# Kernel optimization log

Measured on AMD Instinct MI355X. Metric: run time of the kernel, lower is better.

Reference implementation:

```python
import jax, jax.numpy as jnp
import numpy as np

INFEAT = 4096
OUTFEAT = 11008
TOKENS = 2048


def setup_inputs() -> dict:
    key = jax.random.key(0)
    k1, k2, k3, k4, k5 = jax.random.split(key, 5)
    x = jax.random.normal(k1, (TOKENS, INFEAT), dtype=jnp.float32)
    # Random uint8 int-weights, packed 4-per-uint32 exactly like pack():
    # word = w1 | w2<<8 | w3<<16 | w4<<24, rows grouped along infeatures.
    wbytes = jax.random.randint(k2, (INFEAT // 4, 4, OUTFEAT), 0, 256, dtype=jnp.int32).astype(jnp.uint32)
    qweight = (wbytes[:, 0] | (wbytes[:, 1] << 8) | (wbytes[:, 2] << 16) | (wbytes[:, 3] << 24))
    qweight = qweight.astype(jnp.int32)  # same bit pattern as uint32 buffer
    scales = (jax.random.uniform(k3, (OUTFEAT,), dtype=jnp.float32) * 0.01 + 1e-4)
    zeros = jax.random.randint(k4, (OUTFEAT,), 0, 256, dtype=jnp.int32)  # uint8 zero points
    bias = jax.random.normal(k5, (OUTFEAT,), dtype=jnp.float32) * 0.01
    return {"x": x, "qweight": qweight, "scales": scales, "zeros": zeros, "bias": bias}


def _dequant(qweight, scales, zeros):
    q = qweight.astype(jnp.uint32)  # [INFEAT//4, OUTFEAT]
    b0 = (q & 0xFF)
    b1 = ((q >> 8) & 0xFF)
    b2 = ((q >> 16) & 0xFF)
    b3 = ((q >> 24) & 0xFF)
    w_int = jnp.stack([b0, b1, b2, b3], axis=1).reshape(-1, q.shape[-1])  # [INFEAT, OUTFEAT]
    # pack(): int = round(w/scale) + zero  =>  w = (int - zero) * scale (per output channel)
    return (w_int.astype(jnp.float32) - zeros.astype(jnp.float32)[None, :]) * scales[None, :]


def reference(x, qweight, scales, zeros, bias):
    w = _dequant(qweight, scales, zeros)          # [INFEAT, OUTFEAT]
    return x @ w + bias[None, :]                  # [TOKENS, OUTFEAT]
```

## Files before the change

kernel.cpp:

```cpp
#include <hip/hip_runtime.h>
#include <hip/hip_bf16.h>

#define INFEAT 4096
#define OUTFEAT 11008
#define TOKENS 2048

typedef int v4i __attribute__((ext_vector_type(4)));
typedef __bf16 bf16_t;
typedef bf16_t bf16x4 __attribute__((ext_vector_type(4)));
typedef bf16_t bf16x8 __attribute__((ext_vector_type(8)));
typedef float f32x4 __attribute__((ext_vector_type(4)));

__device__ __forceinline__ void async_copy16(const void* g, void* l) {
    __builtin_amdgcn_global_load_lds((const __attribute__((address_space(1))) void*)g,
                                     (__attribute__((address_space(3))) void*)l,
                                     16, 0, 0);
}

__global__ __launch_bounds__(256) void quant_x(
    const float* __restrict__ x, unsigned int* __restrict__ xq,
    float* __restrict__ xscale, int* __restrict__ xsum)
{
    __shared__ float smax[4];
    __shared__ int ssum[4];
    const int row = blockIdx.x;
    const int tid = threadIdx.x;
    const int lane = tid & 63, wid = tid >> 6;
    const float* xr = x + (size_t)row * INFEAT;

    float4 v[4];
    #pragma unroll
    for (int i = 0; i < 4; ++i) v[i] = *(const float4*)&xr[tid * 16 + i * 4];

    float am = 0.f;
    #pragma unroll
    for (int i = 0; i < 4; ++i)
        am = fmaxf(am, fmaxf(fmaxf(fabsf(v[i].x), fabsf(v[i].y)),
                             fmaxf(fabsf(v[i].z), fabsf(v[i].w))));
    #pragma unroll
    for (int o = 32; o > 0; o >>= 1) am = fmaxf(am, __shfl_xor(am, o, 64));
    if (lane == 0) smax[wid] = am;
    __syncthreads();
    am = fmaxf(fmaxf(smax[0], smax[1]), fmaxf(smax[2], smax[3]));
    const float inv = am > 0.f ? 127.0f / am : 0.f;
    const float sc  = am > 0.f ? am / 127.0f : 0.f;

    int lsum = 0;
    unsigned int pk[4];
    #pragma unroll
    for (int i = 0; i < 4; ++i) {
        int q0 = (int)rintf(fminf(fmaxf(v[i].x * inv, -127.f), 127.f));
        int q1 = (int)rintf(fminf(fmaxf(v[i].y * inv, -127.f), 127.f));
        int q2 = (int)rintf(fminf(fmaxf(v[i].z * inv, -127.f), 127.f));
        int q3 = (int)rintf(fminf(fmaxf(v[i].w * inv, -127.f), 127.f));
        lsum += q0 + q1 + q2 + q3;
        pk[i] = (q0 & 255) | ((q1 & 255) << 8) | ((q2 & 255) << 16) | ((unsigned)(q3 & 255) << 24);
    }
    *(uint4*)&xq[(size_t)row * (INFEAT / 4) + tid * 4] = *(uint4*)pk;

    #pragma unroll
    for (int o = 32; o > 0; o >>= 1) lsum += __shfl_xor(lsum, o, 64);
    if (lane == 0) ssum[wid] = lsum;
    __syncthreads();
    if (tid == 0) {
        xsum[row] = ssum[0] + ssum[1] + ssum[2] + ssum[3];
        xscale[row] = sc;
    }
}

__global__ __launch_bounds__(256) void t_w(
    const unsigned int* __restrict__ qw, unsigned char* __restrict__ wt)
{
    __shared__ unsigned int Tw[64 * 64];
    const int n0 = blockIdx.x * 64;
    const int kp0 = blockIdx.y * 64;
    const int tn = threadIdx.x & 63;
    const int tk4 = threadIdx.x >> 6;

    #pragma unroll
    for (int it = 0; it < 16; ++it) {
        const int kp = tk4 * 16 + it;
        const unsigned int q = qw[(size_t)(kp0 + kp) * OUTFEAT + n0 + tn] ^ 0x80808080u;
        const int slot = (kp >> 2) ^ (tn & 15);
        Tw[tn * 64 + slot * 4 + (kp & 3)] = q;
    }
    __syncthreads();

    #pragma unroll
    for (int i = 0; i < 4; ++i) {
        const int flat = i * 256 + threadIdx.x;
        const int n = flat >> 4;
        const int c = flat & 15;
        uint4 v = *(const uint4*)&Tw[n * 64 + ((c ^ (n & 15)) * 4)];
        *(uint4*)&wt[(size_t)(n0 + n) * INFEAT + (size_t)kp0 * 4 + c * 16] = v;
    }
}

__global__ __launch_bounds__(256, 4) void q3gemm_i8(
    const unsigned char* __restrict__ xqb, const unsigned char* __restrict__ wt,
    const float* __restrict__ scales, const int* __restrict__ zeros,
    const float* __restrict__ bias, const float* __restrict__ xscale,
    const int* __restrict__ xsum, float* __restrict__ out)
{
    __shared__ unsigned char Als[128 * 128];
    __shared__ unsigned char Bls[128 * 128];

    const int tid = threadIdx.x;
    const int n0 = (blockIdx.x >> 4) * 128;
    const int m0 = (blockIdx.x & 15) * 128;

    const int wid = tid >> 6, lane = tid & 63;
    const int wm = (wid & 1) * 64, wn = (wid >> 1) * 64;
    const int lr = lane & 15, lq = lane >> 4;

    const int rb0  = wid * 32;
    const int rsub = lane >> 3;
    const int sl   = lane & 7;

    v4i acc[4][4];
    #pragma unroll
    for (int i = 0; i < 4; ++i)
        #pragma unroll
        for (int j = 0; j < 4; ++j)
            acc[i][j] = (v4i){0, 0, 0, 0};

    for (int kt = 0; kt < INFEAT / 128; ++kt) {
        const int k0 = kt * 128;

        #pragma unroll
        for (int p = 0; p < 4; ++p) {
            const int r = rb0 + p * 8 + rsub;
            const int s = sl ^ (r & 7);
            async_copy16(&xqb[(size_t)(m0 + r) * INFEAT + k0 + s * 16], Als + (rb0 + p * 8) * 128);
        }
        #pragma unroll
        for (int p = 0; p < 4; ++p) {
            const int r = rb0 + p * 8 + rsub;
            const int s = sl ^ (r & 7);
            async_copy16(&wt[(size_t)(n0 + r) * INFEAT + k0 + s * 16], Bls + (rb0 + p * 8) * 128);
        }

        __syncthreads();

        #pragma unroll
        for (int ks = 0; ks < 2; ++ks) {
            v4i af[4], bfv[4];
            #pragma unroll
            for (int t = 0; t < 4; ++t) {
                const int ra = wm + t * 16 + lr;
                const int pa = (ks * 4 + lq) ^ (ra & 7);
                af[t] = *(const v4i*)&Als[ra * 128 + pa * 16];
                const int rb = wn + t * 16 + lr;
                const int pb = (ks * 4 + lq) ^ (rb & 7);
                bfv[t] = *(const v4i*)&Bls[rb * 128 + pb * 16];
            }
            #pragma unroll
            for (int i = 0; i < 4; ++i)
                #pragma unroll
                for (int j = 0; j < 4; ++j)
                    acc[i][j] = __builtin_amdgcn_mfma_i32_16x16x64_i8(af[i], bfv[j], acc[i][j], 0, 0, 0);
        }

        __syncthreads();
    }

    #pragma unroll
    for (int j = 0; j < 4; ++j) {
        const int col = n0 + wn + j * 16 + lr;
        const float sn = scales[col];
        const int zi = 128 - zeros[col];
        const float bv = bias[col];
        #pragma unroll
        for (int i = 0; i < 4; ++i) {
            const int rb = m0 + wm + i * 16 + lq * 4;
            #pragma unroll
            for (int r = 0; r < 4; ++r) {
                const int tot = acc[i][j][r] + zi * xsum[rb + r];
                out[(size_t)(rb + r) * OUTFEAT + col] = xscale[rb + r] * sn * (float)tot + bv;
            }
        }
    }
}

#define LDSS 72
__global__ __launch_bounds__(256) void q3gemm_fb(
    const float* __restrict__ x, const unsigned int* __restrict__ qw,
    const float* __restrict__ scales, const int* __restrict__ zeros,
    const float* __restrict__ bias, float* __restrict__ out)
{
    __shared__ bf16_t Als[128 * LDSS];
    __shared__ bf16_t Bls[128 * LDSS];
    const int tid = threadIdx.x;
    const int m0 = blockIdx.y * 128;
    const int n0 = blockIdx.x * 128;
    const int bcol = tid & 127;
    const int bpr  = tid >> 7;
    const float scf = scales[n0 + bcol];
    const float nzs = (float)zeros[n0 + bcol] * scf;
    const int acolg = tid & 15;
    const int arow0 = tid >> 4;
    const int wid  = tid >> 6;
    const int lane = tid & 63;
    const int wm = (wid & 1) * 64;
    const int wn = (wid >> 1) * 64;
    const int lr = lane & 15;
    const int lq = lane >> 4;
    f32x4 acc[4][4];
    #pragma unroll
    for (int i = 0; i < 4; ++i)
        #pragma unroll
        for (int j = 0; j < 4; ++j) acc[i][j] = (f32x4)0.0f;
    for (int kt = 0; kt < INFEAT / 64; ++kt) {
        const int k0 = kt * 64;
        #pragma unroll
        for (int p = 0; p < 8; ++p) {
            const int row = arow0 + p * 16;
            const float4 v = *(const float4*)&x[(size_t)(m0 + row) * INFEAT + k0 + acolg * 4];
            bf16x4 b;
            b[0] = (bf16_t)v.x; b[1] = (bf16_t)v.y; b[2] = (bf16_t)v.z; b[3] = (bf16_t)v.w;
            *(bf16x4*)&Als[row * LDSS + acolg * 4] = b;
        }
        const int kp0 = k0 >> 2;
        #pragma unroll
        for (int it = 0; it < 8; ++it) {
            const int prel = it * 2 + bpr;
            const unsigned int q = qw[(size_t)(kp0 + prel) * OUTFEAT + n0 + bcol];
            bf16x4 b;
            b[0] = (bf16_t)((float)(q & 0xFFu)        * scf - nzs);
            b[1] = (bf16_t)((float)((q >> 8) & 0xFFu) * scf - nzs);
            b[2] = (bf16_t)((float)((q >> 16) & 0xFFu)* scf - nzs);
            b[3] = (bf16_t)((float)(q >> 24)          * scf - nzs);
            *(bf16x4*)&Bls[bcol * LDSS + prel * 4] = b;
        }
        __syncthreads();
        #pragma unroll
        for (int ks = 0; ks < 2; ++ks) {
            bf16x8 af[4], bfv[4];
            #pragma unroll
            for (int t = 0; t < 4; ++t) {
                af[t]  = *(const bf16x8*)&Als[(wm + t * 16 + lr) * LDSS + ks * 32 + lq * 8];
                bfv[t] = *(const bf16x8*)&Bls[(wn + t * 16 + lr) * LDSS + ks * 32 + lq * 8];
            }
            #pragma unroll
            for (int i = 0; i < 4; ++i)
                #pragma unroll
                for (int j = 0; j < 4; ++j)
                    acc[i][j] = __builtin_amdgcn_mfma_f32_16x16x32_bf16(af[i], bfv[j], acc[i][j], 0, 0, 0);
        }
        __syncthreads();
    }
    #pragma unroll
    for (int j = 0; j < 4; ++j) {
        const int col = n0 + wn + j * 16 + lr;
        const float bv = bias[col];
        #pragma unroll
        for (int i = 0; i < 4; ++i) {
            const int rbs = m0 + wm + i * 16 + lq * 4;
            #pragma unroll
            for (int r = 0; r < 4; ++r)
                out[(size_t)(rbs + r) * OUTFEAT + col] = acc[i][j][r] + bv;
        }
    }
}

extern "C" void kernel_launch(void* const* d_in, const int* in_sizes, int n_in,
                              void* d_out, int out_size, void* d_ws, size_t ws_size,
                              hipStream_t stream) {
    const float*        x      = (const float*)d_in[0];
    const unsigned int* qw     = (const unsigned int*)d_in[1];
    const float*        scales = (const float*)d_in[2];
    const int*          zeros  = (const int*)d_in[3];
    const float*        bias   = (const float*)d_in[4];
    float*              out    = (float*)d_out;

    const size_t wt_bytes = (size_t)OUTFEAT * INFEAT;
    const size_t xq_bytes = (size_t)TOKENS * INFEAT;
    const size_t need = wt_bytes + xq_bytes + TOKENS * (sizeof(float) + sizeof(int)) + 256;

    if (ws_size >= need) {
        unsigned char* wt = (unsigned char*)d_ws;
        unsigned int* xq  = (unsigned int*)((char*)d_ws + wt_bytes);
        float* xscale = (float*)((char*)d_ws + wt_bytes + xq_bytes);
        int*   xsum   = (int*)((char*)d_ws + wt_bytes + xq_bytes + TOKENS * sizeof(float));

        quant_x<<<dim3(TOKENS), dim3(256), 0, stream>>>(x, xq, xscale, xsum);
        t_w<<<dim3(OUTFEAT / 64, (INFEAT / 4) / 64), dim3(256), 0, stream>>>(qw, wt);
        q3gemm_i8<<<dim3((OUTFEAT / 128) * (TOKENS / 128)), dim3(256), 0, stream>>>(
            (const unsigned char*)xq, wt, scales, zeros, bias, xscale, xsum, out);
    } else {
        q3gemm_fb<<<dim3(OUTFEAT / 128, TOKENS / 128), dim3(256), 0, stream>>>(
            x, qw, scales, zeros, bias, out);
    }
}
```

Baseline: 297.6 us.

## Fuse prep kernels and triple-buffer a 256x128 int8 MFMA GEMM

Merges the activation quantization and weight transpose into one launch, and the transpose now reads with 16-byte loads. The int8 GEMM moves to 512-thread blocks with 256x128 tiles and a three-stage async global-to-LDS pipeline. K-steps are split into phases interleaved with prefetches, with explicit waitcnt, barriers and setprio. This aims to hide load latency and cut launch overhead, at the cost of much more LDS per block (144KB), lower occupancy and fragile hand-written synchronisation.

```diff
diff --git a/kernel.cpp b/kernel.cpp
--- a/kernel.cpp
+++ b/kernel.cpp
@@ -17,151 +17,227 @@
                                      16, 0, 0);
 }
 
-__global__ __launch_bounds__(256) void quant_x(
-    const float* __restrict__ x, unsigned int* __restrict__ xq,
-    float* __restrict__ xscale, int* __restrict__ xsum)
+__global__ __launch_bounds__(256) void prep(
+    const float* __restrict__ x, const unsigned int* __restrict__ qw,
+    unsigned int* __restrict__ xq, float* __restrict__ xscale, int* __restrict__ xsum,
+    unsigned char* __restrict__ wt)
 {
+    __shared__ unsigned int Tw[64 * 64];
     __shared__ float smax[4];
     __shared__ int ssum[4];
-    const int row = blockIdx.x;
     const int tid = threadIdx.x;
-    const int lane = tid & 63, wid = tid >> 6;
-    const float* xr = x + (size_t)row * INFEAT;
-
-    float4 v[4];
-    #pragma unroll
-    for (int i = 0; i < 4; ++i) v[i] = *(const float4*)&xr[tid * 16 + i * 4];
-
-    float am = 0.f;
-    #pragma unroll
-    for (int i = 0; i < 4; ++i)
-        am = fmaxf(am, fmaxf(fmaxf(fabsf(v[i].x), fabsf(v[i].y)),
-                             fmaxf(fabsf(v[i].z), fabsf(v[i].w))));
-    #pragma unroll
-    for (int o = 32; o > 0; o >>= 1) am = fmaxf(am, __shfl_xor(am, o, 64));
-    if (lane == 0) smax[wid] = am;
-    __syncthreads();
-    am = fmaxf(fmaxf(smax[0], smax[1]), fmaxf(smax[2], smax[3]));
-    const float inv = am > 0.f ? 127.0f / am : 0.f;
-    const float sc  = am > 0.f ? am / 127.0f : 0.f;
-
-    int lsum = 0;
-    unsigned int pk[4];
-    #pragma unroll
-    for (int i = 0; i < 4; ++i) {
-        int q0 = (int)rintf(fminf(fmaxf(v[i].x * inv, -127.f), 127.f));
-        int q1 = (int)rintf(fminf(fmaxf(v[i].y * inv, -127.f), 127.f));
-        int q2 = (int)rintf(fminf(fmaxf(v[i].z * inv, -127.f), 127.f));
-        int q3 = (int)rintf(fminf(fmaxf(v[i].w * inv, -127.f), 127.f));
-        lsum += q0 + q1 + q2 + q3;
-        pk[i] = (q0 & 255) | ((q1 & 255) << 8) | ((q2 & 255) << 16) | ((unsigned)(q3 & 255) << 24);
-    }
-    *(uint4*)&xq[(size_t)row * (INFEAT / 4) + tid * 4] = *(uint4*)pk;
-
-    #pragma unroll
-    for (int o = 32; o > 0; o >>= 1) lsum += __shfl_xor(lsum, o, 64);
-    if (lane == 0) ssum[wid] = lsum;
-    __syncthreads();
-    if (tid == 0) {
-        xsum[row] = ssum[0] + ssum[1] + ssum[2] + ssum[3];
-        xscale[row] = sc;
-    }
-}
-
-__global__ __launch_bounds__(256) void t_w(
-    const unsigned int* __restrict__ qw, unsigned char* __restrict__ wt)
-{
-    __shared__ unsigned int Tw[64 * 64];
-    const int n0 = blockIdx.x * 64;
-    const int kp0 = blockIdx.y * 64;
-    const int tn = threadIdx.x & 63;
-    const int tk4 = threadIdx.x >> 6;
-
-    #pragma unroll
-    for (int it = 0; it < 16; ++it) {
-        const int kp = tk4 * 16 + it;
-        const unsigned int q = qw[(size_t)(kp0 + kp) * OUTFEAT + n0 + tn] ^ 0x80808080u;
-        const int slot = (kp >> 2) ^ (tn & 15);
-        Tw[tn * 64 + slot * 4 + (kp & 3)] = q;
-    }
-    __syncthreads();
-
-    #pragma unroll
-    for (int i = 0; i < 4; ++i) {
-        const int flat = i * 256 + threadIdx.x;
-        const int n = flat >> 4;
-        const int c = flat & 15;
-        uint4 v = *(const uint4*)&Tw[n * 64 + ((c ^ (n & 15)) * 4)];
-        *(uint4*)&wt[(size_t)(n0 + n) * INFEAT + (size_t)kp0 * 4 + c * 16] = v;
-    }
-}
-
-__global__ __launch_bounds__(256, 4) void q3gemm_i8(
+
+    if (blockIdx.x < 2752) {
+        const int bid = blockIdx.x;
+        const int n0  = (bid % 172) * 64;
+        const int kp0 = (bid / 172) * 64;
+        const int tn4 = tid & 15;
+        const int kb  = tid >> 4;
+        #pragma unroll
+        for (int it = 0; it < 4; ++it) {
+            const int kp = kb + it * 16;
+            uint4 q = *(const uint4*)&qw[(size_t)(kp0 + kp) * OUTFEAT + n0 + tn4 * 4];
+            q.x ^= 0x80808080u; q.y ^= 0x80808080u; q.z ^= 0x80808080u; q.w ^= 0x80808080u;
+            const int ks = kp >> 2, kq = kp & 3;
+            const int n = tn4 * 4;
+            Tw[(n + 0) * 64 + ((ks ^ ((n + 0) & 15)) << 2) + kq] = q.x;
+            Tw[(n + 1) * 64 + ((ks ^ ((n + 1) & 15)) << 2) + kq] = q.y;
+            Tw[(n + 2) * 64 + ((ks ^ ((n + 2) & 15)) << 2) + kq] = q.z;
+            Tw[(n + 3) * 64 + ((ks ^ ((n + 3) & 15)) << 2) + kq] = q.w;
+        }
+        __syncthreads();
+        #pragma unroll
+        for (int i = 0; i < 4; ++i) {
+            const int flat = i * 256 + tid;
+            const int n = flat >> 4;
+            const int c = flat & 15;
+            uint4 v = *(const uint4*)&Tw[n * 64 + ((c ^ (n & 15)) * 4)];
+            *(uint4*)&wt[(size_t)(n0 + n) * INFEAT + (size_t)kp0 * 4 + c * 16] = v;
+        }
+    } else {
+        const int row = blockIdx.x - 2752;
+        const int lane = tid & 63, wid = tid >> 6;
+        const float* xr = x + (size_t)row * INFEAT;
+
+        float4 v[4];
+        #pragma unroll
+        for (int i = 0; i < 4; ++i) v[i] = *(const float4*)&xr[tid * 16 + i * 4];
+
+        float am = 0.f;
+        #pragma unroll
+        for (int i = 0; i < 4; ++i)
+            am = fmaxf(am, fmaxf(fmaxf(fabsf(v[i].x), fabsf(v[i].y)),
+                                 fmaxf(fabsf(v[i].z), fabsf(v[i].w))));
+        #pragma unroll
+        for (int o = 32; o > 0; o >>= 1) am = fmaxf(am, __shfl_xor(am, o, 64));
+        if (lane == 0) smax[wid] = am;
+        __syncthreads();
+        am = fmaxf(fmaxf(smax[0], smax[1]), fmaxf(smax[2], smax[3]));
+        const float inv = am > 0.f ? 127.0f / am : 0.f;
+        const float sc  = am > 0.f ? am / 127.0f : 0.f;
+
+        int lsum = 0;
+        unsigned int pk[4];
+        #pragma unroll
+        for (int i = 0; i < 4; ++i) {
+            int q0 = (int)rintf(fminf(fmaxf(v[i].x * inv, -127.f), 127.f));
+            int q1 = (int)rintf(fminf(fmaxf(v[i].y * inv, -127.f), 127.f));
+            int q2 = (int)rintf(fminf(fmaxf(v[i].z * inv, -127.f), 127.f));
+            int q3 = (int)rintf(fminf(fmaxf(v[i].w * inv, -127.f), 127.f));
+            lsum += q0 + q1 + q2 + q3;
+            pk[i] = (q0 & 255) | ((q1 & 255) << 8) | ((q2 & 255) << 16) | ((unsigned)(q3 & 255) << 24);
+        }
+        *(uint4*)&xq[(size_t)row * (INFEAT / 4) + tid * 4] = *(uint4*)pk;
+
+        #pragma unroll
+        for (int o = 32; o > 0; o >>= 1) lsum += __shfl_xor(lsum, o, 64);
+        if (lane == 0) ssum[wid] = lsum;
+        __syncthreads();
+        if (tid == 0) {
+            xsum[row] = ssum[0] + ssum[1] + ssum[2] + ssum[3];
+            xscale[row] = sc;
+        }
+    }
+}
+
+#define MFMA_I8(d, a, b) d = __builtin_amdgcn_mfma_i32_16x16x64_i8(a, b, d, 0, 0, 0)
+
+__global__ __launch_bounds__(512, 2) void q3gemm_i8p(
     const unsigned char* __restrict__ xqb, const unsigned char* __restrict__ wt,
     const float* __restrict__ scales, const int* __restrict__ zeros,
     const float* __restrict__ bias, const float* __restrict__ xscale,
     const int* __restrict__ xsum, float* __restrict__ out)
 {
-    __shared__ unsigned char Als[128 * 128];
-    __shared__ unsigned char Bls[128 * 128];
-
-    const int tid = threadIdx.x;
-    const int n0 = (blockIdx.x >> 4) * 128;
-    const int m0 = (blockIdx.x & 15) * 128;
-
-    const int wid = tid >> 6, lane = tid & 63;
-    const int wm = (wid & 1) * 64, wn = (wid >> 1) * 64;
+    __shared__ unsigned char Als[3][256 * 128];
+    __shared__ unsigned char Bls[3][128 * 128];
+
+    const int tid  = threadIdx.x;
+    const int wid  = tid >> 6, lane = tid & 63;
+    const int m0 = (blockIdx.x & 7) * 256;
+    const int n0 = (blockIdx.x >> 3) * 128;
+    const int wm = (wid & 3) * 64;
+    const int wn = (wid >> 2) * 64;
     const int lr = lane & 15, lq = lane >> 4;
-
-    const int rb0  = wid * 32;
-    const int rsub = lane >> 3;
-    const int sl   = lane & 7;
+    const int rsub = lane >> 3, sl = lane & 7;
+
+    const unsigned char* aSrc = xqb + (size_t)m0 * INFEAT;
+    const unsigned char* bSrc = wt  + (size_t)n0 * INFEAT;
 
     v4i acc[4][4];
     #pragma unroll
     for (int i = 0; i < 4; ++i)
         #pragma unroll
-        for (int j = 0; j < 4; ++j)
-            acc[i][j] = (v4i){0, 0, 0, 0};
-
-    for (int kt = 0; kt < INFEAT / 128; ++kt) {
-        const int k0 = kt * 128;
-
-        #pragma unroll
-        for (int p = 0; p < 4; ++p) {
-            const int r = rb0 + p * 8 + rsub;
-            const int s = sl ^ (r & 7);
-            async_copy16(&xqb[(size_t)(m0 + r) * INFEAT + k0 + s * 16], Als + (rb0 + p * 8) * 128);
-        }
-        #pragma unroll
-        for (int p = 0; p < 4; ++p) {
-            const int r = rb0 + p * 8 + rsub;
-            const int s = sl ^ (r & 7);
-            async_copy16(&wt[(size_t)(n0 + r) * INFEAT + k0 + s * 16], Bls + (rb0 + p * 8) * 128);
-        }
-
-        __syncthreads();
-
-        #pragma unroll
-        for (int ks = 0; ks < 2; ++ks) {
-            v4i af[4], bfv[4];
-            #pragma unroll
-            for (int t = 0; t < 4; ++t) {
-                const int ra = wm + t * 16 + lr;
-                const int pa = (ks * 4 + lq) ^ (ra & 7);
-                af[t] = *(const v4i*)&Als[ra * 128 + pa * 16];
-                const int rb = wn + t * 16 + lr;
-                const int pb = (ks * 4 + lq) ^ (rb & 7);
-                bfv[t] = *(const v4i*)&Bls[rb * 128 + pb * 16];
-            }
-            #pragma unroll
-            for (int i = 0; i < 4; ++i)
-                #pragma unroll
-                for (int j = 0; j < 4; ++j)
-                    acc[i][j] = __builtin_amdgcn_mfma_i32_16x16x64_i8(af[i], bfv[j], acc[i][j], 0, 0, 0);
-        }
-
-        __syncthreads();
+        for (int j = 0; j < 4; ++j) acc[i][j] = (v4i){0, 0, 0, 0};
+
+#define STAGE_A(T, C, P) do {                                                        \
+    const int r_ = wid * 32 + (P) * 8 + rsub;                                        \
+    const int s_ = sl ^ (r_ & 7);                                                    \
+    async_copy16(&aSrc[(size_t)r_ * INFEAT + (T) * 128 + s_ * 16],                   \
+                 &Als[C][(wid * 32 + (P) * 8) * 128]);                               \
+} while (0)
+#define STAGE_B(T, C, P) do {                                                        \
+    const int r_ = wid * 16 + (P) * 8 + rsub;                                        \
+    const int s_ = sl ^ (r_ & 7);                                                    \
+    async_copy16(&bSrc[(size_t)r_ * INFEAT + (T) * 128 + s_ * 16],                   \
+                 &Bls[C][(wid * 16 + (P) * 8) * 128]);                               \
+} while (0)
+
+    STAGE_A(0, 0, 0); STAGE_A(0, 0, 1); STAGE_A(0, 0, 2); STAGE_A(0, 0, 3);
+    STAGE_B(0, 0, 0); STAGE_B(0, 0, 1);
+    STAGE_A(1, 1, 0); STAGE_A(1, 1, 1); STAGE_A(1, 1, 2); STAGE_A(1, 1, 3);
+    STAGE_B(1, 1, 0); STAGE_B(1, 1, 1);
+    asm volatile("s_waitcnt vmcnt(6)" ::: "memory");
+    __builtin_amdgcn_s_barrier();
+
+    const int NT = INFEAT / 128;
+    int c = 0;
+    for (int t = 0; t < NT; ++t) {
+        const int cn = (c >= 1) ? c - 1 : 2;
+        const unsigned char* Ab = Als[c];
+        const unsigned char* Bb = Bls[c];
+        const bool pf = (t + 2 < NT);
+        v4i af0, af1, af2, af3, bf0, bf1, bf2, bf3;
+
+        {
+            const int ra0 = wm + lr,      ra1 = wm + 16 + lr;
+            af0 = *(const v4i*)&Ab[ra0 * 128 + (lq ^ (ra0 & 7)) * 16];
+            af1 = *(const v4i*)&Ab[ra1 * 128 + (lq ^ (ra1 & 7)) * 16];
+            const int rb0 = wn + lr,      rb1 = wn + 16 + lr;
+            const int rb2 = wn + 32 + lr, rb3 = wn + 48 + lr;
+            bf0 = *(const v4i*)&Bb[rb0 * 128 + (lq ^ (rb0 & 7)) * 16];
+            bf1 = *(const v4i*)&Bb[rb1 * 128 + (lq ^ (rb1 & 7)) * 16];
+            bf2 = *(const v4i*)&Bb[rb2 * 128 + (lq ^ (rb2 & 7)) * 16];
+            bf3 = *(const v4i*)&Bb[rb3 * 128 + (lq ^ (rb3 & 7)) * 16];
+            if (pf) { STAGE_A(t + 2, cn, 0); STAGE_A(t + 2, cn, 1); }
+            __builtin_amdgcn_s_barrier();
+            asm volatile("s_waitcnt lgkmcnt(0)" ::: "memory");
+            __builtin_amdgcn_sched_barrier(0);
+            __builtin_amdgcn_s_setprio(1);
+            MFMA_I8(acc[0][0], af0, bf0); MFMA_I8(acc[0][1], af0, bf1);
+            MFMA_I8(acc[0][2], af0, bf2); MFMA_I8(acc[0][3], af0, bf3);
+            MFMA_I8(acc[1][0], af1, bf0); MFMA_I8(acc[1][1], af1, bf1);
+            MFMA_I8(acc[1][2], af1, bf2); MFMA_I8(acc[1][3], af1, bf3);
+            __builtin_amdgcn_s_setprio(0);
+            __builtin_amdgcn_s_barrier();
+        }
+        {
+            const int ra2 = wm + 32 + lr, ra3 = wm + 48 + lr;
+            af2 = *(const v4i*)&Ab[ra2 * 128 + (lq ^ (ra2 & 7)) * 16];
+            af3 = *(const v4i*)&Ab[ra3 * 128 + (lq ^ (ra3 & 7)) * 16];
+            if (pf) { STAGE_A(t + 2, cn, 2); STAGE_A(t + 2, cn, 3); }
+            __builtin_amdgcn_s_barrier();
+            asm volatile("s_waitcnt lgkmcnt(0)" ::: "memory");
+            __builtin_amdgcn_sched_barrier(0);
+            __builtin_amdgcn_s_setprio(1);
+            MFMA_I8(acc[2][0], af2, bf0); MFMA_I8(acc[2][1], af2, bf1);
+            MFMA_I8(acc[2][2], af2, bf2); MFMA_I8(acc[2][3], af2, bf3);
+            MFMA_I8(acc[3][0], af3, bf0); MFMA_I8(acc[3][1], af3, bf1);
+            MFMA_I8(acc[3][2], af3, bf2); MFMA_I8(acc[3][3], af3, bf3);
+            __builtin_amdgcn_s_setprio(0);
+            __builtin_amdgcn_s_barrier();
+        }
+        {
+            const int ra0 = wm + lr,      ra1 = wm + 16 + lr;
+            af0 = *(const v4i*)&Ab[ra0 * 128 + ((4 + lq) ^ (ra0 & 7)) * 16];
+            af1 = *(const v4i*)&Ab[ra1 * 128 + ((4 + lq) ^ (ra1 & 7)) * 16];
+            const int rb0 = wn + lr,      rb1 = wn + 16 + lr;
+            const int rb2 = wn + 32 + lr, rb3 = wn + 48 + lr;
+            bf0 = *(const v4i*)&Bb[rb0 * 128 + ((4 + lq) ^ (rb0 & 7)) * 16];
+            bf1 = *(const v4i*)&Bb[rb1 * 128 + ((4 + lq) ^ (rb1 & 7)) * 16];
+            bf2 = *(const v4i*)&Bb[rb2 * 128 + ((4 + lq) ^ (rb2 & 7)) * 16];
+            bf3 = *(const v4i*)&Bb[rb3 * 128 + ((4 + lq) ^ (rb3 & 7)) * 16];
+            if (pf) { STAGE_B(t + 2, cn, 0); }
+            __builtin_amdgcn_s_barrier();
+            asm volatile("s_waitcnt lgkmcnt(0)" ::: "memory");
+            __builtin_amdgcn_sched_barrier(0);
+            __builtin_amdgcn_s_setprio(1);
+            MFMA_I8(acc[0][0], af0, bf0); MFMA_I8(acc[0][1], af0, bf1);
+            MFMA_I8(acc[0][2], af0, bf2); MFMA_I8(acc[0][3], af0, bf3);
+            MFMA_I8(acc[1][0], af1, bf0); MFMA_I8(acc[1][1], af1, bf1);
+            MFMA_I8(acc[1][2], af1, bf2); MFMA_I8(acc[1][3], af1, bf3);
+            __builtin_amdgcn_s_setprio(0);
+            __builtin_amdgcn_s_barrier();
+        }
+        {
+            const int ra2 = wm + 32 + lr, ra3 = wm + 48 + lr;
+            af2 = *(const v4i*)&Ab[ra2 * 128 + ((4 + lq) ^ (ra2 & 7)) * 16];
+            af3 = *(const v4i*)&Ab[ra3 * 128 + ((4 + lq) ^ (ra3 & 7)) * 16];
+            if (pf) { STAGE_B(t + 2, cn, 1); }
+            __builtin_amdgcn_s_barrier();
+            asm volatile("s_waitcnt lgkmcnt(0)" ::: "memory");
+            __builtin_amdgcn_sched_barrier(0);
+            __builtin_amdgcn_s_setprio(1);
+            MFMA_I8(acc[2][0], af2, bf0); MFMA_I8(acc[2][1], af2, bf1);
+            MFMA_I8(acc[2][2], af2, bf2); MFMA_I8(acc[2][3], af2, bf3);
+            MFMA_I8(acc[3][0], af3, bf0); MFMA_I8(acc[3][1], af3, bf1);
+            MFMA_I8(acc[3][2], af3, bf2); MFMA_I8(acc[3][3], af3, bf3);
+            __builtin_amdgcn_s_setprio(0);
+            if (t < NT - 2) { asm volatile("s_waitcnt vmcnt(6)" ::: "memory"); }
+            else            { asm volatile("s_waitcnt vmcnt(0)" ::: "memory"); }
+            __builtin_amdgcn_sched_barrier(0);
+            __builtin_amdgcn_s_barrier();
+        }
+        c = (c == 2) ? 0 : c + 1;
     }
 
     #pragma unroll
@@ -180,6 +256,8 @@
             }
         }
     }
+#undef STAGE_A
+#undef STAGE_B
 }
 
 #define LDSS 72
@@ -283,9 +361,8 @@
         float* xscale = (float*)((char*)d_ws + wt_bytes + xq_bytes);
         int*   xsum   = (int*)((char*)d_ws + wt_bytes + xq_bytes + TOKENS * sizeof(float));
 
-        quant_x<<<dim3(TOKENS), dim3(256), 0, stream>>>(x, xq, xscale, xsum);
-        t_w<<<dim3(OUTFEAT / 64, (INFEAT / 4) / 64), dim3(256), 0, stream>>>(qw, wt);
-        q3gemm_i8<<<dim3((OUTFEAT / 128) * (TOKENS / 128)), dim3(256), 0, stream>>>(
+        prep<<<dim3(2752 + TOKENS), dim3(256), 0, stream>>>(x, qw, xq, xscale, xsum, wt);
+        q3gemm_i8p<<<dim3((OUTFEAT / 128) * (TOKENS / 256)), dim3(512), 0, stream>>>(
             (const unsigned char*)xq, wt, scales, zeros, bias, xscale, xsum, out);
     } else {
         q3gemm_fb<<<dim3(OUTFEAT / 128, TOKENS / 128), dim3(256), 0, stream>>>(
```

After: 303.7 us. 2.1% more time.
